# Kernel tuning notes

Hardware: AMD Instinct MI355X
Metric: run time of the kernel (lower is better)

## Reference

```python
import jax, jax.numpy as jnp
import numpy as np

CAUSAL = True


def setup_inputs() -> dict:
    key = jax.random.key(0)
    k1, k2, k3 = jax.random.split(key, 3)
    B, S, D_IN, D_INNER, D_OUT = 4, 4096, 512, 64, 512
    x = jax.random.normal(k1, (B, S, D_IN), dtype=jnp.float32)
    W_qkv = jax.random.normal(k2, (D_IN, 3 * D_INNER), dtype=jnp.float32) * (D_IN ** -0.5)
    W_out = jax.random.normal(k3, (D_INNER, D_OUT), dtype=jnp.float32) * (D_INNER ** -0.5)
    b_out = jnp.zeros((D_OUT,), dtype=jnp.float32)
    return {"x": x, "W_qkv": W_qkv, "W_out": W_out, "b_out": b_out}


def reference(x, W_qkv, W_out, b_out):
    d_inner = W_out.shape[0]
    scale = d_inner ** -0.5
    qkv = jnp.einsum('bsi,io->bso', x, W_qkv)  # [B,S,3*d_inner]
    q, k, v = jnp.split(qkv, 3, axis=-1)
    sim = jnp.einsum('bid,bjd->bij', q, k) * scale  # [B,S,S]
    if CAUSAL:
        S = x.shape[1]
        mask = jnp.triu(jnp.ones((S, S), dtype=bool), k=1)
        sim = jnp.where(mask[None], -jnp.finfo(q.dtype).max, sim)
    attn = jax.nn.softmax(sim, axis=-1)
    out = jnp.einsum('bij,bjd->bid', attn, v)  # [B,S,d_inner]
    return jnp.einsum('bid,do->bio', out, W_out) + b_out
```

## Files before the change

kernel.cpp:

```cpp
#include <hip/hip_runtime.h>
#include <math.h>

typedef __attribute__((ext_vector_type(8))) short short8;
typedef __attribute__((ext_vector_type(4))) short short4v;
typedef __attribute__((ext_vector_type(4))) float f32x4;
typedef __attribute__((ext_vector_type(4))) float float4v;
typedef __attribute__((ext_vector_type(2))) unsigned int uint2v;

__device__ __forceinline__ unsigned short f2bf(float f){
  unsigned int u = __float_as_uint(f);
  u += 0x7FFFu + ((u >> 16) & 1u);
  return (unsigned short)(u >> 16);
}
__device__ __forceinline__ float bf2f(short s){
  return __uint_as_float(((unsigned int)(unsigned short)s) << 16);
}
__device__ __forceinline__ unsigned int cvtpk(float lo, float hi){
  unsigned int r;
  asm("v_cvt_pk_bf16_f32 %0, %1, %2" : "=v"(r) : "v"(lo), "v"(hi));
  return r;
}

typedef __attribute__((address_space(1))) const unsigned char* gas_t;
typedef __attribute__((address_space(3))) unsigned char* las_t;
__device__ __forceinline__ void async16(const void* g, void* l) {
  __builtin_amdgcn_global_load_lds((gas_t)g, (las_t)l, 16, 0, 0);
}

#define SC2 0.1803368801111204f

__global__ __launch_bounds__(256) void prep_w(
    const float* __restrict__ Wqkv, const float* __restrict__ Wout,
    unsigned short* __restrict__ Wtq, unsigned short* __restrict__ Wto)
{
  int idx = blockIdx.x * 256 + threadIdx.x;
  if (idx < 192 * 512) {
    int n = idx >> 9, k = idx & 511;
    Wtq[idx] = f2bf(Wqkv[k * 192 + n]);
  } else {
    int i2 = idx - 192 * 512;
    int n = i2 >> 6, k = i2 & 63;
    Wto[i2] = f2bf(Wout[k * 512 + n]);
  }
}

__global__ __launch_bounds__(256) void qkv_kernel(
    const float* __restrict__ x,
    const unsigned short* __restrict__ Wt,
    unsigned short* __restrict__ qg,
    unsigned short* __restrict__ kg,
    unsigned short* __restrict__ vT)
{
  __shared__ __align__(16) unsigned short Wb[64][128];
  __shared__ __align__(16) unsigned short vbuf[64][72];
  const int part = blockIdx.x % 3;
  const int rb   = blockIdx.x / 3;
  const int lane = threadIdx.x & 63;
  const int wave = threadIdx.x >> 6;
  const int mrow = lane & 15;
  const int quad = lane >> 4;
  const int mb = rb * 64;
  const int m0 = mb + wave * 16;
  const int sw = mrow & 7;

  const int srow = lane >> 4;
  const int sch  = lane & 15;
#define STAGE_W(s)                                                            \
  {                                                                           \
    _Pragma("unroll")                                                         \
    for (int ii = 0; ii < 4; ii++) {                                          \
      const int r0 = wave * 16 + ii * 4;                                      \
      const int r  = r0 + srow;                                               \
      const int cd = (sch & 8) | ((sch ^ (r & 7)) & 7);                       \
      async16(Wt + (size_t)(part * 64 + r) * 512 + (s) * 128 + cd * 8,        \
              &Wb[r0][0]);                                                    \
    }                                                                         \
  }

  STAGE_W(0)

  f32x4 acc[4];
#pragma unroll
  for (int t = 0; t < 4; t++) acc[t] = (f32x4){0.f, 0.f, 0.f, 0.f};
  const float* xp = x + (size_t)(m0 + mrow) * 512 + quad * 8;

  for (int s = 0; s < 4; s++) {
    __syncthreads();
#pragma unroll
    for (int l = 0; l < 4; l++) {
      const int kk = s * 4 + l;
      float4v a0 = *(const float4v*)(xp + kk * 32);
      float4v a1 = *(const float4v*)(xp + kk * 32 + 4);
      short8 af;
#pragma unroll
      for (int j = 0; j < 4; j++) { af[j] = (short)f2bf(a0[j]); af[4 + j] = (short)f2bf(a1[j]); }
      const int c   = l * 4 + quad;
      const int pos = (c & 8) | ((c ^ sw) & 7);
#pragma unroll
      for (int t = 0; t < 4; t++) {
        short8 bf = *(const short8*)(&Wb[t * 16 + mrow][0] + pos * 8);
        acc[t] = __builtin_amdgcn_mfma_f32_16x16x32_bf16(af, bf, acc[t], 0, 0, 0);
      }
    }
    __syncthreads();
    if (s < 3) STAGE_W(s + 1)
  }

  const float osc = (part == 0) ? SC2 : 1.0f;
#pragma unroll
  for (int t = 0; t < 4; t++)
#pragma unroll
    for (int r = 0; r < 4; r++)
      vbuf[wave * 16 + quad * 4 + r][t * 16 + mrow] = f2bf(acc[t][r] * osc);
  __syncthreads();

  if (part < 2) {
    unsigned short* dst = part ? kg : qg;
    const int row = threadIdx.x >> 2;
    const int seg = (threadIdx.x & 3) * 16;
    short8 w0 = *(const short8*)&vbuf[row][seg];
    short8 w1 = *(const short8*)&vbuf[row][seg + 8];
    unsigned short* p = dst + (size_t)(mb + row) * 64 + seg;
    *(short8*)(p) = w0;
    *(short8*)(p + 8) = w1;
  } else {
    const int d  = threadIdx.x >> 2;
    const int s8 = (threadIdx.x & 3) * 16;
    const int bb = rb >> 6;
    const int sb = mb & 4095;
    short8 w0, w1;
#pragma unroll
    for (int i = 0; i < 8; i++) {
      w0[i] = (short)vbuf[s8 + i][d];
      w1[i] = (short)vbuf[s8 + 8 + i][d];
    }
    unsigned short* dst = vT + (size_t)bb * (64 * 4096) + (size_t)d * 4096 + sb + s8;
    *(short8*)(dst) = w0;
    *(short8*)(dst + 8) = w1;
  }
#undef STAGE_W
}

template <bool MASKED>
__device__ __forceinline__ void soft_pv(
    const f32x4* sA, const short8* vf, int kb, int qlane, int quad, int mrow,
    float& lacc, f32x4* o, unsigned short (*pb)[72])
{
  float p[16];
#pragma unroll
  for (int t = 0; t < 4; t++)
#pragma unroll
    for (int r = 0; r < 4; r++) {
      float v = sA[t][r];
      if (MASKED && (kb + t * 16 + quad * 4 + r > qlane)) v = -3.0e38f;
      p[t * 4 + r] = exp2f(v);
    }
  float ps = 0.f;
#pragma unroll
  for (int i = 0; i < 16; i++) ps += p[i];
  lacc += ps;
#pragma unroll
  for (int t = 0; t < 4; t++) {
    unsigned int d0 = cvtpk(p[t * 4 + 0], p[t * 4 + 1]);
    unsigned int d1 = cvtpk(p[t * 4 + 2], p[t * 4 + 3]);
    *(uint2v*)&pb[mrow][t * 16 + quad * 4] = (uint2v){d0, d1};
  }
  short8 pf0 = *(const short8*)&pb[mrow][quad * 8];
  short8 pf1 = *(const short8*)&pb[mrow][32 + quad * 8];
#pragma unroll
  for (int c = 0; c < 4; c++) {
    o[c] = __builtin_amdgcn_mfma_f32_16x16x32_bf16(vf[2 * c],     pf0, o[c], 0, 0, 0);
    o[c] = __builtin_amdgcn_mfma_f32_16x16x32_bf16(vf[2 * c + 1], pf1, o[c], 0, 0, 0);
  }
}

__global__ __launch_bounds__(512) void attn_kernel(
    const unsigned short* __restrict__ qg,
    const unsigned short* __restrict__ kg,
    const unsigned short* __restrict__ vT,
    unsigned short* __restrict__ Opart,
    float* __restrict__ lpart)
{
  __shared__ __align__(16) unsigned short Kb[2][64][64];
  __shared__ __align__(16) unsigned short Vb[2][64][64];
  __shared__ __align__(16) unsigned short pbuf[8][16][72];
  const int lane = threadIdx.x & 63;
  const int wave = threadIdx.x >> 6;
  const int mrow = lane & 15;
  const int quad = lane >> 4;
  const int sw   = mrow & 7;

  int t = 143 - (blockIdx.x % 144);
  const int b = blockIdx.x / 144;
  int qj = 31, c = 0;
  for (int qq = 0; qq < 32; qq++) {
    const int ncq = (qq >> 2) + 1;
    if (t < ncq) { qj = qq; c = t; break; }
    t -= ncq;
  }

  const int sq0w = qj * 128 + wave * 16;
  const int g0w  = b * 4096 + sq0w;

  short8 qf[2];
  {
    const unsigned short* qp = qg + (size_t)(g0w + mrow) * 64 + quad * 8;
    qf[0] = *(const short8*)(qp);
    qf[1] = *(const short8*)(qp + 32);
  }

  const int kstart = c << 9;
  const int qend   = qj * 128 + 128;
  const int kend   = (kstart + 512 < qend) ? (kstart + 512) : qend;
  const int nTb    = (kend - kstart) >> 6;

  f32x4 o[4];
#pragma unroll
  for (int ct = 0; ct < 4; ct++) o[ct] = (f32x4){0.f, 0.f, 0.f, 0.f};
  float lr = 0.f;

  const unsigned short* kbase = kg + (size_t)b * 4096 * 64;
  const unsigned short* vbase = vT + (size_t)b * 64 * 4096;
  const int shalf = lane >> 3;
  const int sch   = lane & 7;

#define STAGE_KV(kb, Kd, Vd)                                                  \
  {                                                                           \
    const int r0 = wave * 8;                                                  \
    const int r  = r0 + shalf;                                                \
    const int cd = sch ^ (r & 7);                                             \
    async16(kbase + (size_t)((kb) + r) * 64 + cd * 8, (Kd) + r0 * 64);        \
    async16(vbase + (size_t)r * 4096 + (kb) + cd * 8, (Vd) + r0 * 64);        \
  }

  STAGE_KV(kstart, &Kb[0][0][0], &Vb[0][0][0])
  __syncthreads();

  for (int j = 0; j < nTb; j++) {
    const int kb = kstart + 64 * j;
    if (j + 1 < nTb)
      STAGE_KV(kb + 64, &Kb[(j + 1) & 1][0][0], &Vb[(j + 1) & 1][0][0])
    const unsigned short* Kc = &Kb[j & 1][0][0];
    const unsigned short* Vc = &Vb[j & 1][0][0];

    const bool act = (kb <= sq0w + 15);
    if (act) {
      short8 kf[8];
#pragma unroll
      for (int tt = 0; tt < 4; tt++) {
        const unsigned short* kr = Kc + (tt * 16 + mrow) * 64;
        kf[2 * tt]     = *(const short8*)(kr + (quad ^ sw) * 8);
        kf[2 * tt + 1] = *(const short8*)(kr + ((quad + 4) ^ sw) * 8);
      }
      f32x4 sA[4];
#pragma unroll
      for (int tt = 0; tt < 4; tt++) {
        f32x4 z = (f32x4){0.f, 0.f, 0.f, 0.f};
        z = __builtin_amdgcn_mfma_f32_16x16x32_bf16(kf[2 * tt],     qf[0], z, 0, 0, 0);
        z = __builtin_amdgcn_mfma_f32_16x16x32_bf16(kf[2 * tt + 1], qf[1], z, 0, 0, 0);
        sA[tt] = z;
      }
      short8 vf[8];
#pragma unroll
      for (int cc = 0; cc < 4; cc++) {
        const unsigned short* vr = Vc + (cc * 16 + mrow) * 64;
        vf[2 * cc]     = *(const short8*)(vr + (quad ^ sw) * 8);
        vf[2 * cc + 1] = *(const short8*)(vr + ((quad + 4) ^ sw) * 8);
      }
      if (kb + 63 <= sq0w)
        soft_pv<false>(sA, vf, kb, sq0w + mrow, quad, mrow, lr, o, pbuf[wave]);
      else
        soft_pv<true> (sA, vf, kb, sq0w + mrow, quad, mrow, lr, o, pbuf[wave]);
    }
    __syncthreads();
  }
#undef STAGE_KV

  {
    float lt = lr;
    lt += __shfl_xor(lt, 16);
    lt += __shfl_xor(lt, 32);
    const size_t row = (size_t)c * 16384 + g0w + mrow;
#pragma unroll
    for (int ct = 0; ct < 4; ct++) {
      short4v ob;
#pragma unroll
      for (int r = 0; r < 4; r++) ob[r] = (short)f2bf(o[ct][r]);
      *(short4v*)(Opart + row * 64 + ct * 16 + quad * 4) = ob;
    }
    if (quad == 0) lpart[row] = lt;
  }
}

__global__ __launch_bounds__(256) void combine_kernel(
    const unsigned short* __restrict__ Opart,
    const float* __restrict__ lpart,
    const unsigned short* __restrict__ WtO,
    const float* __restrict__ bias,
    float* __restrict__ out)
{
  __shared__ __align__(16) unsigned short Wob[128][64];
  __shared__ __align__(16) float obuf[4][16][132];
  const int lane = threadIdx.x & 63;
  const int wave = threadIdx.x >> 6;
  const int mrow = lane & 15;
  const int quad = lane >> 4;
  const int rb = blockIdx.x >> 2;
  const int ch = blockIdx.x & 3;
  const int g0 = rb * 64 + wave * 16;
  const int nc = ((g0 & 4095) >> 9) + 1;

  {
    const int half = lane >> 3;
    const int chp  = lane & 7;
#pragma unroll
    for (int ii = 0; ii < 4; ii++) {
      const int r0 = wave * 32 + ii * 8;
      const int r  = r0 + half;
      const int cd = chp ^ (r & 7);
      async16(WtO + (size_t)(ch * 128 + r) * 64 + cd * 8, &Wob[r0][0]);
    }
  }

  float L = 0.f;
  f32x4 A0 = (f32x4){0,0,0,0}, A1 = A0, A2 = A0, A3 = A0;
  for (int cI = 0; cI < nc; cI++) {
    const size_t row = (size_t)cI * 16384 + g0 + mrow;
    L += lpart[row];
    const unsigned short* op = Opart + row * 64 + quad * 8;
    short8 x0 = *(const short8*)(op);
    short8 x1 = *(const short8*)(op + 32);
#pragma unroll
    for (int j = 0; j < 4; j++) {
      A0[j] += bf2f(x0[j]); A1[j] += bf2f(x0[4 + j]);
      A2[j] += bf2f(x1[j]); A3[j] += bf2f(x1[4 + j]);
    }
  }
  const float inv = 1.0f / L;
  short8 of0, of1;
#pragma unroll
  for (int i = 0; i < 4; i++) {
    of0[i]     = (short)f2bf(A0[i] * inv);
    of0[i + 4] = (short)f2bf(A1[i] * inv);
    of1[i]     = (short)f2bf(A2[i] * inv);
    of1[i + 4] = (short)f2bf(A3[i] * inv);
  }
  __syncthreads();

  const int sw = mrow & 7;
#pragma unroll
  for (int t = 0; t < 8; t++) {
    const int n = ch * 128 + t * 16 + mrow;
    const unsigned short* wr = &Wob[t * 16 + mrow][0];
    short8 w0 = *(const short8*)(wr + (quad ^ sw) * 8);
    short8 w1 = *(const short8*)(wr + ((quad + 4) ^ sw) * 8);
    f32x4 pr = (f32x4){0,0,0,0};
    pr = __builtin_amdgcn_mfma_f32_16x16x32_bf16(of0, w0, pr, 0, 0, 0);
    pr = __builtin_amdgcn_mfma_f32_16x16x32_bf16(of1, w1, pr, 0, 0, 0);
    const float bv = bias[n];
#pragma unroll
    for (int r = 0; r < 4; r++)
      obuf[wave][quad * 4 + r][t * 16 + mrow] = pr[r] + bv;
  }
#pragma unroll
  for (int j = 0; j < 4; j++) {
#pragma unroll
    for (int h = 0; h < 2; h++) {
      const int row = 4 * j + (lane >> 4);
      const int col = 4 * (lane & 15) + 64 * h;
      float4v v = *(const float4v*)&obuf[wave][row][col];
      *(float4v*)(out + (size_t)(g0 + row) * 512 + ch * 128 + col) = v;
    }
  }
}

extern "C" void kernel_launch(void* const* d_in, const int* in_sizes, int n_in,
                              void* d_out, int out_size, void* d_ws, size_t ws_size,
                              hipStream_t stream) {
  const float* x    = (const float*)d_in[0];
  const float* Wqkv = (const float*)d_in[1];
  const float* Wout = (const float*)d_in[2];
  const float* bout = (const float*)d_in[3];
  float* out = (float*)d_out;

  unsigned short* q   = (unsigned short*)d_ws;
  unsigned short* k   = q   + 16384 * 64;
  unsigned short* vT  = k   + 16384 * 64;
  unsigned short* Wtq = vT  + 4 * 64 * 4096;
  unsigned short* Wto = Wtq + 192 * 512;
  unsigned short* Opart = Wto + 512 * 64;
  float* lprt = (float*)(Opart + (size_t)8 * 16384 * 64);

  prep_w<<<512, 256, 0, stream>>>(Wqkv, Wout, Wtq, Wto);
  qkv_kernel<<<768, 256, 0, stream>>>(x, Wtq, q, k, vT);
  attn_kernel<<<576, 512, 0, stream>>>(q, k, vT, Opart, lprt);
  combine_kernel<<<1024, 256, 0, stream>>>(Opart, lprt, Wto, bout, out);
}
```

Measured before the change: 143.3 us.

## Fuse split-K combine and output projection into attention kernel via completion counters

Removes the separate combine kernel. Each attention block increments a per-query-tile atomic counter, and the last block to finish for that tile reduces the partial outputs and row sums, then applies the output projection with bias, reading W_out directly from global memory. Counters are zeroed inside the qkv kernel, and shared memory is unioned so the output staging buffer reuses the K/V buffers. This saves one launch and the combine kernel's scheduling, at the cost of serialized tail work in the last-finishing blocks, uncached weight reads, and an occupancy hint of 4 blocks per CU in launch bounds.

```diff
diff --git a/kernel.cpp b/kernel.cpp
--- a/kernel.cpp
+++ b/kernel.cpp
@@ -49,8 +49,11 @@
     const unsigned short* __restrict__ Wt,
     unsigned short* __restrict__ qg,
     unsigned short* __restrict__ kg,
-    unsigned short* __restrict__ vT)
+    unsigned short* __restrict__ vT,
+    unsigned int* __restrict__ cnt)
 {
+  if (blockIdx.x == 0 && threadIdx.x < 128) cnt[threadIdx.x] = 0;
+
   __shared__ __align__(16) unsigned short Wb[64][128];
   __shared__ __align__(16) unsigned short vbuf[64][72];
   const int part = blockIdx.x % 3;
@@ -174,16 +177,25 @@
   }
 }
 
-__global__ __launch_bounds__(512) void attn_kernel(
+__global__ __launch_bounds__(512, 4) void attn_kernel(
     const unsigned short* __restrict__ qg,
     const unsigned short* __restrict__ kg,
     const unsigned short* __restrict__ vT,
     unsigned short* __restrict__ Opart,
-    float* __restrict__ lpart)
+    float* __restrict__ lpart,
+    const unsigned short* __restrict__ WtO,
+    const float* __restrict__ bias,
+    float* __restrict__ out,
+    unsigned int* __restrict__ cnt)
 {
-  __shared__ __align__(16) unsigned short Kb[2][64][64];
-  __shared__ __align__(16) unsigned short Vb[2][64][64];
-  __shared__ __align__(16) unsigned short pbuf[8][16][72];
+  __shared__ __align__(16) unsigned char smem[67584];
+  __shared__ int fin;
+  unsigned short* Kbase = (unsigned short*)smem;
+  unsigned short* Vbase = Kbase + 8192;
+  unsigned short (*pbufw)[72] =
+      (unsigned short (*)[72])(smem + 32768);
+  float* obuf = (float*)smem;
+
   const int lane = threadIdx.x & 63;
   const int wave = threadIdx.x >> 6;
   const int mrow = lane & 15;
@@ -233,15 +245,15 @@
     async16(vbase + (size_t)r * 4096 + (kb) + cd * 8, (Vd) + r0 * 64);        \
   }
 
-  STAGE_KV(kstart, &Kb[0][0][0], &Vb[0][0][0])
+  STAGE_KV(kstart, Kbase, Vbase)
   __syncthreads();
 
   for (int j = 0; j < nTb; j++) {
     const int kb = kstart + 64 * j;
     if (j + 1 < nTb)
-      STAGE_KV(kb + 64, &Kb[(j + 1) & 1][0][0], &Vb[(j + 1) & 1][0][0])
-    const unsigned short* Kc = &Kb[j & 1][0][0];
-    const unsigned short* Vc = &Vb[j & 1][0][0];
+      STAGE_KV(kb + 64, Kbase + ((j + 1) & 1) * 4096, Vbase + ((j + 1) & 1) * 4096)
+    const unsigned short* Kc = Kbase + (j & 1) * 4096;
+    const unsigned short* Vc = Vbase + (j & 1) * 4096;
 
     const bool act = (kb <= sq0w + 15);
     if (act) {
@@ -268,9 +280,9 @@
         vf[2 * cc + 1] = *(const short8*)(vr + ((quad + 4) ^ sw) * 8);
       }
       if (kb + 63 <= sq0w)
-        soft_pv<false>(sA, vf, kb, sq0w + mrow, quad, mrow, lr, o, pbuf[wave]);
+        soft_pv<false>(sA, vf, kb, sq0w + mrow, quad, mrow, lr, o, pbufw + wave * 16);
       else
-        soft_pv<true> (sA, vf, kb, sq0w + mrow, quad, mrow, lr, o, pbuf[wave]);
+        soft_pv<true> (sA, vf, kb, sq0w + mrow, quad, mrow, lr, o, pbufw + wave * 16);
     }
     __syncthreads();
   }
@@ -290,42 +302,22 @@
     }
     if (quad == 0) lpart[row] = lt;
   }
-}
-
-__global__ __launch_bounds__(256) void combine_kernel(
-    const unsigned short* __restrict__ Opart,
-    const float* __restrict__ lpart,
-    const unsigned short* __restrict__ WtO,
-    const float* __restrict__ bias,
-    float* __restrict__ out)
-{
-  __shared__ __align__(16) unsigned short Wob[128][64];
-  __shared__ __align__(16) float obuf[4][16][132];
-  const int lane = threadIdx.x & 63;
-  const int wave = threadIdx.x >> 6;
-  const int mrow = lane & 15;
-  const int quad = lane >> 4;
-  const int rb = blockIdx.x >> 2;
-  const int ch = blockIdx.x & 3;
-  const int g0 = rb * 64 + wave * 16;
-  const int nc = ((g0 & 4095) >> 9) + 1;
-
-  {
-    const int half = lane >> 3;
-    const int chp  = lane & 7;
-#pragma unroll
-    for (int ii = 0; ii < 4; ii++) {
-      const int r0 = wave * 32 + ii * 8;
-      const int r  = r0 + half;
-      const int cd = chp ^ (r & 7);
-      async16(WtO + (size_t)(ch * 128 + r) * 64 + cd * 8, &Wob[r0][0]);
-    }
-  }
-
+
+  __syncthreads();
+  __threadfence();
+  if (threadIdx.x == 0) {
+    unsigned int old = atomicAdd(&cnt[b * 32 + qj], 1u);
+    fin = (old == (unsigned)(qj >> 2));
+  }
+  __syncthreads();
+  if (!fin) return;
+  __threadfence();
+
+  const int nch = (qj >> 2) + 1;
   float L = 0.f;
   f32x4 A0 = (f32x4){0,0,0,0}, A1 = A0, A2 = A0, A3 = A0;
-  for (int cI = 0; cI < nc; cI++) {
-    const size_t row = (size_t)cI * 16384 + g0 + mrow;
+  for (int cI = 0; cI < nch; cI++) {
+    const size_t row = (size_t)cI * 16384 + g0w + mrow;
     L += lpart[row];
     const unsigned short* op = Opart + row * 64 + quad * 8;
     short8 x0 = *(const short8*)(op);
@@ -347,29 +339,31 @@
   }
   __syncthreads();
 
-  const int sw = mrow & 7;
-#pragma unroll
-  for (int t = 0; t < 8; t++) {
-    const int n = ch * 128 + t * 16 + mrow;
-    const unsigned short* wr = &Wob[t * 16 + mrow][0];
-    short8 w0 = *(const short8*)(wr + (quad ^ sw) * 8);
-    short8 w1 = *(const short8*)(wr + ((quad + 4) ^ sw) * 8);
-    f32x4 pr = (f32x4){0,0,0,0};
-    pr = __builtin_amdgcn_mfma_f32_16x16x32_bf16(of0, w0, pr, 0, 0, 0);
-    pr = __builtin_amdgcn_mfma_f32_16x16x32_bf16(of1, w1, pr, 0, 0, 0);
-    const float bv = bias[n];
-#pragma unroll
-    for (int r = 0; r < 4; r++)
-      obuf[wave][quad * 4 + r][t * 16 + mrow] = pr[r] + bv;
-  }
-#pragma unroll
-  for (int j = 0; j < 4; j++) {
-#pragma unroll
-    for (int h = 0; h < 2; h++) {
-      const int row = 4 * j + (lane >> 4);
-      const int col = 4 * (lane & 15) + 64 * h;
-      float4v v = *(const float4v*)&obuf[wave][row][col];
-      *(float4v*)(out + (size_t)(g0 + row) * 512 + ch * 128 + col) = v;
+  float* obw = obuf + wave * 16 * 132;
+  for (int ch = 0; ch < 4; ch++) {
+#pragma unroll
+    for (int t8 = 0; t8 < 8; t8++) {
+      const int n = ch * 128 + t8 * 16 + mrow;
+      const unsigned short* wr = WtO + (size_t)n * 64;
+      short8 w0 = *(const short8*)(wr + quad * 8);
+      short8 w1 = *(const short8*)(wr + quad * 8 + 32);
+      f32x4 pr = (f32x4){0,0,0,0};
+      pr = __builtin_amdgcn_mfma_f32_16x16x32_bf16(of0, w0, pr, 0, 0, 0);
+      pr = __builtin_amdgcn_mfma_f32_16x16x32_bf16(of1, w1, pr, 0, 0, 0);
+      const float bv = bias[n];
+#pragma unroll
+      for (int r = 0; r < 4; r++)
+        obw[(quad * 4 + r) * 132 + t8 * 16 + mrow] = pr[r] + bv;
+    }
+#pragma unroll
+    for (int j = 0; j < 4; j++) {
+#pragma unroll
+      for (int h = 0; h < 2; h++) {
+        const int row = 4 * j + (lane >> 4);
+        const int col = 4 * (lane & 15) + 64 * h;
+        float4v v = *(const float4v*)&obw[row * 132 + col];
+        *(float4v*)(out + (size_t)(g0w + row) * 512 + ch * 128 + col) = v;
+      }
     }
   }
 }
@@ -390,9 +384,9 @@
   unsigned short* Wto = Wtq + 192 * 512;
   unsigned short* Opart = Wto + 512 * 64;
   float* lprt = (float*)(Opart + (size_t)8 * 16384 * 64);
+  unsigned int* cnt = (unsigned int*)(lprt + 8 * 16384);
 
   prep_w<<<512, 256, 0, stream>>>(Wqkv, Wout, Wtq, Wto);
-  qkv_kernel<<<768, 256, 0, stream>>>(x, Wtq, q, k, vT);
-  attn_kernel<<<576, 512, 0, stream>>>(q, k, vT, Opart, lprt);
-  combine_kernel<<<1024, 256, 0, stream>>>(Opart, lprt, Wto, bout, out);
-}
+  qkv_kernel<<<768, 256, 0, stream>>>(x, Wtq, q, k, vT, cnt);
+  attn_kernel<<<576, 512, 0, stream>>>(q, k, vT, Opart, lprt, Wto, bout, out, cnt);
+}
```

Measured after the change: 354.2 us. 147% more time.

## Load K/V fragments directly from global memory, dropping LDS staging and barriers

Applied to the files above, without the earlier changes.

Removes the double-buffered async LDS staging of K and V tiles and the per-iteration block barrier. Each wave now reads its K and V MFMA fragments straight from global memory (through the cache), and stops early with a break once its query rows are fully masked. This cuts the LDS traffic and lets waves run without synchronising. The cost is that the eight waves each fetch the same tiles redundantly, and global-load latency is no longer hidden by prefetching.

```diff
diff --git a/kernel.cpp b/kernel.cpp
--- a/kernel.cpp
+++ b/kernel.cpp
@@ -181,14 +181,11 @@
     unsigned short* __restrict__ Opart,
     float* __restrict__ lpart)
 {
-  __shared__ __align__(16) unsigned short Kb[2][64][64];
-  __shared__ __align__(16) unsigned short Vb[2][64][64];
   __shared__ __align__(16) unsigned short pbuf[8][16][72];
   const int lane = threadIdx.x & 63;
   const int wave = threadIdx.x >> 6;
   const int mrow = lane & 15;
   const int quad = lane >> 4;
-  const int sw   = mrow & 7;
 
   int t = 143 - (blockIdx.x % 144);
   const int b = blockIdx.x / 144;
@@ -221,60 +218,38 @@
 
   const unsigned short* kbase = kg + (size_t)b * 4096 * 64;
   const unsigned short* vbase = vT + (size_t)b * 64 * 4096;
-  const int shalf = lane >> 3;
-  const int sch   = lane & 7;
-
-#define STAGE_KV(kb, Kd, Vd)                                                  \
-  {                                                                           \
-    const int r0 = wave * 8;                                                  \
-    const int r  = r0 + shalf;                                                \
-    const int cd = sch ^ (r & 7);                                             \
-    async16(kbase + (size_t)((kb) + r) * 64 + cd * 8, (Kd) + r0 * 64);        \
-    async16(vbase + (size_t)r * 4096 + (kb) + cd * 8, (Vd) + r0 * 64);        \
-  }
-
-  STAGE_KV(kstart, &Kb[0][0][0], &Vb[0][0][0])
-  __syncthreads();
 
   for (int j = 0; j < nTb; j++) {
     const int kb = kstart + 64 * j;
-    if (j + 1 < nTb)
-      STAGE_KV(kb + 64, &Kb[(j + 1) & 1][0][0], &Vb[(j + 1) & 1][0][0])
-    const unsigned short* Kc = &Kb[j & 1][0][0];
-    const unsigned short* Vc = &Vb[j & 1][0][0];
-
-    const bool act = (kb <= sq0w + 15);
-    if (act) {
-      short8 kf[8];
-#pragma unroll
-      for (int tt = 0; tt < 4; tt++) {
-        const unsigned short* kr = Kc + (tt * 16 + mrow) * 64;
-        kf[2 * tt]     = *(const short8*)(kr + (quad ^ sw) * 8);
-        kf[2 * tt + 1] = *(const short8*)(kr + ((quad + 4) ^ sw) * 8);
-      }
-      f32x4 sA[4];
-#pragma unroll
-      for (int tt = 0; tt < 4; tt++) {
-        f32x4 z = (f32x4){0.f, 0.f, 0.f, 0.f};
-        z = __builtin_amdgcn_mfma_f32_16x16x32_bf16(kf[2 * tt],     qf[0], z, 0, 0, 0);
-        z = __builtin_amdgcn_mfma_f32_16x16x32_bf16(kf[2 * tt + 1], qf[1], z, 0, 0, 0);
-        sA[tt] = z;
-      }
-      short8 vf[8];
-#pragma unroll
-      for (int cc = 0; cc < 4; cc++) {
-        const unsigned short* vr = Vc + (cc * 16 + mrow) * 64;
-        vf[2 * cc]     = *(const short8*)(vr + (quad ^ sw) * 8);
-        vf[2 * cc + 1] = *(const short8*)(vr + ((quad + 4) ^ sw) * 8);
-      }
-      if (kb + 63 <= sq0w)
-        soft_pv<false>(sA, vf, kb, sq0w + mrow, quad, mrow, lr, o, pbuf[wave]);
-      else
-        soft_pv<true> (sA, vf, kb, sq0w + mrow, quad, mrow, lr, o, pbuf[wave]);
-    }
-    __syncthreads();
-  }
-#undef STAGE_KV
+    if (kb > sq0w + 15) break;
+
+    short8 kf[8];
+#pragma unroll
+    for (int tt = 0; tt < 4; tt++) {
+      const unsigned short* kr = kbase + (size_t)(kb + tt * 16 + mrow) * 64;
+      kf[2 * tt]     = *(const short8*)(kr + quad * 8);
+      kf[2 * tt + 1] = *(const short8*)(kr + quad * 8 + 32);
+    }
+    f32x4 sA[4];
+#pragma unroll
+    for (int tt = 0; tt < 4; tt++) {
+      f32x4 z = (f32x4){0.f, 0.f, 0.f, 0.f};
+      z = __builtin_amdgcn_mfma_f32_16x16x32_bf16(kf[2 * tt],     qf[0], z, 0, 0, 0);
+      z = __builtin_amdgcn_mfma_f32_16x16x32_bf16(kf[2 * tt + 1], qf[1], z, 0, 0, 0);
+      sA[tt] = z;
+    }
+    short8 vf[8];
+#pragma unroll
+    for (int cc = 0; cc < 4; cc++) {
+      const unsigned short* vr = vbase + (size_t)(cc * 16 + mrow) * 4096 + kb;
+      vf[2 * cc]     = *(const short8*)(vr + quad * 8);
+      vf[2 * cc + 1] = *(const short8*)(vr + quad * 8 + 32);
+    }
+    if (kb + 63 <= sq0w)
+      soft_pv<false>(sA, vf, kb, sq0w + mrow, quad, mrow, lr, o, pbuf[wave]);
+    else
+      soft_pv<true> (sA, vf, kb, sq0w + mrow, quad, mrow, lr, o, pbuf[wave]);
+  }
 
   {
     float lt = lr;
```

Measured after the change: 200.8 us. 40.1% more time.
